# Optimization experiments

Measured on AMD Instinct MI355X. Metric: run time of the kernel, lower is better.

Reference implementation:

```python
import jax, jax.numpy as jnp
import numpy as np

N, E, IN, H, OUT = 100000, 1600000, 128, 128, 64


def setup_inputs() -> dict:
    key = jax.random.key(0)
    ks = jax.random.split(key, 7)
    x = jax.random.normal(ks[0], (N, IN), dtype=jnp.float32)
    edge_index = jax.random.randint(ks[1], (2, E), 0, N, dtype=jnp.int32)
    # Glorot-style scaled params (PyG SAGEConv: lin_l has bias, lin_r does not)
    s1 = 1.0 / np.sqrt(IN)
    s2 = 1.0 / np.sqrt(H)
    W1_l = jax.random.normal(ks[2], (H, IN), dtype=jnp.float32) * s1
    W1_r = jax.random.normal(ks[3], (H, IN), dtype=jnp.float32) * s1
    b1 = jnp.zeros((H,), dtype=jnp.float32)
    W2_l = jax.random.normal(ks[4], (OUT, H), dtype=jnp.float32) * s2
    W2_r = jax.random.normal(ks[5], (OUT, H), dtype=jnp.float32) * s2
    b2 = jnp.zeros((OUT,), dtype=jnp.float32)
    return {"x": x, "W1_l": W1_l, "W1_r": W1_r, "b1": b1,
            "W2_l": W2_l, "W2_r": W2_r, "b2": b2, "edge_index": edge_index}


def _sage_conv(x, edge_index, W_l, W_r, b):
    # mean-aggregate source-node features at target nodes, then linear + root term
    src, dst = edge_index[0], edge_index[1]
    n = x.shape[0]
    msgs = x[src]                                                   # [E, d]
    agg = jax.ops.segment_sum(msgs, dst, num_segments=n)            # [N, d]
    deg = jax.ops.segment_sum(jnp.ones((src.shape[0],), x.dtype), dst, num_segments=n)
    mean = agg / jnp.clip(deg, 1.0)[:, None]                        # zero-deg nodes stay 0
    return mean @ W_l.T + b + x @ W_r.T


def reference(x, W1_l, W1_r, b1, W2_l, W2_r, b2, edge_index):
    h = _sage_conv(x, edge_index, W1_l, W1_r, b1)
    h = jax.nn.relu(h)  # dropout p=0.0 -> identity
    out = _sage_conv(h, edge_index, W2_l, W2_r, b2)
    return out
```

## Files before the change

### kernel.cpp

```cpp
#include <hip/hip_runtime.h>


typedef unsigned int uint32;
typedef short bf16x4 __attribute__((ext_vector_type(4)));
typedef short bf16x8 __attribute__((ext_vector_type(8)));
typedef float f32x16 __attribute__((ext_vector_type(16)));

__device__ __forceinline__ uint32 pack_bf16_rne(float a, float b) {
    uint32 ua = __float_as_uint(a);
    uint32 ub = __float_as_uint(b);
    uint32 ra = (ua + 0x7fffu + ((ua >> 16) & 1u)) >> 16;
    uint32 rb = (ub + 0x7fffu + ((ub >> 16) & 1u)) >> 16;
    return ra | (rb << 16);
}
__device__ __forceinline__ float bf_lo(uint32 v) { return __uint_as_float(v << 16); }
__device__ __forceinline__ float bf_hi(uint32 v) { return __uint_as_float(v & 0xffff0000u); }

__device__ __forceinline__ short rne16(float v, float* back) {
    uint32 u = __float_as_uint(v);
    uint32 r = (u + 0x7fffu + ((u >> 16) & 1u)) >> 16;
    *back = __uint_as_float(r << 16);
    return (short)r;
}

__global__ void k_prep(const float* __restrict__ x, uint32* __restrict__ xb,
                       short* __restrict__ xpH, long n4, int spl,
                       const float* __restrict__ W1l, const float* __restrict__ W1r,
                       const float* __restrict__ W2l, const float* __restrict__ W2r,
                       short* __restrict__ W1pH, short* __restrict__ W1pL,
                       short* __restrict__ W2pH, short* __restrict__ W2pL) {
    long i = (long)blockIdx.x * blockDim.x + threadIdx.x;
    float back;
    if (i < n4) {
        int node = (int)(i >> 5);
        int k4 = ((int)i & 31) * 4;
        float4 v = ((const float4*)x)[i];
        bf16x4 hi4;
        hi4[0] = rne16(v.x, &back);
        hi4[1] = rne16(v.y, &back);
        hi4[2] = rne16(v.z, &back);
        hi4[3] = rne16(v.w, &back);
        uint2 o;
        o.x = (uint32)(unsigned short)hi4[0] | ((uint32)(unsigned short)hi4[1] << 16);
        o.y = (uint32)(unsigned short)hi4[2] | ((uint32)(unsigned short)hi4[3] << 16);
        ((uint2*)xb)[i] = o;
        int c = k4 >> 3;
        *(bf16x4*)&xpH[(size_t)c * spl + (size_t)node * 8 + (k4 & 7)] = hi4;
        return;
    }
    int i2 = (int)(i - n4);
    if (i2 < 32768) {
        int j = i2 >> 8, k = i2 & 255;
        float v = (k < 128) ? W1l[j * 128 + k] : W1r[j * 128 + k - 128];
        float hb;
        short hs = rne16(v, &hb);
        short ls = rne16(v - hb, &back);
        int idx = (k >> 3) * 1024 + j * 8 + (k & 7);
        W1pH[idx] = hs;
        W1pL[idx] = ls;
    } else if (i2 < 32768 + 16384) {
        int i3 = i2 - 32768;
        int j = i3 >> 7, k = i3 & 127;
        float v = (j < 64) ? W2l[j * 128 + k] : W2r[(j - 64) * 128 + k];
        float hb;
        short hs = rne16(v, &hb);
        short ls = rne16(v - hb, &back);
        int idx = (k >> 3) * 1024 + j * 8 + (k & 7);
        W2pH[idx] = hs;
        W2pL[idx] = ls;
    }
}


__global__ void k_bcount(const int* __restrict__ ei, int E, int NB,
                         int* __restrict__ bucket_cnt) {
    __shared__ int hist[1024];
    int t = threadIdx.x;
    for (int i = t; i < NB; i += 256) hist[i] = 0;
    __syncthreads();
    int stride = gridDim.x * 256;
    for (int e = blockIdx.x * 256 + t; e < E; e += stride)
        atomicAdd(&hist[ei[E + e] >> 8], 1);
    __syncthreads();
    for (int i = t; i < NB; i += 256) {
        int c = hist[i];
        if (c) atomicAdd(&bucket_cnt[i], c);
    }
}

__global__ void k_bscan(const int* __restrict__ bucket_cnt, int NB, int E,
                        int* __restrict__ bucket_off, int* __restrict__ bucket_cur) {
    __shared__ int s[1024];
    int t = threadIdx.x;
    int v = (t < NB) ? bucket_cnt[t] : 0;
    s[t] = v;
    __syncthreads();
    for (int o = 1; o < 1024; o <<= 1) {
        int u = (t >= o) ? s[t - o] : 0;
        __syncthreads();
        s[t] += u;
        __syncthreads();
    }
    int ex = s[t] - v;
    if (t < NB) { bucket_off[t] = ex; bucket_cur[t] = ex; }
    if (t == NB - 1) bucket_off[NB] = ex + v;
}

__global__ void k_bscatter(const int* __restrict__ ei, int E, int NB,
                           int* __restrict__ bucket_cur, uint32* __restrict__ eb) {
    __shared__ int hist[1024];
    __shared__ int base[1024];
    int t = threadIdx.x;
    for (int i = t; i < NB; i += 256) hist[i] = 0;
    __syncthreads();
    int stride = gridDim.x * 256;
    for (int e = blockIdx.x * 256 + t; e < E; e += stride)
        atomicAdd(&hist[ei[E + e] >> 8], 1);
    __syncthreads();
    for (int i = t; i < NB; i += 256) {
        int c = hist[i];
        base[i] = c ? atomicAdd(&bucket_cur[i], c) : 0;
        hist[i] = 0;
    }
    __syncthreads();
    for (int e = blockIdx.x * 256 + t; e < E; e += stride) {
        int d = ei[E + e];
        int b = d >> 8;
        int r = atomicAdd(&hist[b], 1);
        eb[base[b] + r] = ((uint32)(d & 255) << 24) | (uint32)ei[e];
    }
}

__global__ void k_bfinal(const uint32* __restrict__ eb,
                         const int* __restrict__ bucket_off,
                         int* __restrict__ row_ptr, int* __restrict__ col,
                         int N, int E) {
    __shared__ int deg[256];
    __shared__ int sc[256];
    __shared__ int cur[256];
    int b = blockIdx.x;
    int t = threadIdx.x;
    int beg = bucket_off[b], end = bucket_off[b + 1];
    deg[t] = 0;
    __syncthreads();
    for (int e = beg + t; e < end; e += 256)
        atomicAdd(&deg[eb[e] >> 24], 1);
    __syncthreads();
    int v = deg[t];
    sc[t] = v;
    __syncthreads();
    for (int o = 1; o < 256; o <<= 1) {
        int u = (t >= o) ? sc[t - o] : 0;
        __syncthreads();
        sc[t] += u;
        __syncthreads();
    }
    int ex = sc[t] - v;
    int node = b * 256 + t;
    if (node < N) row_ptr[node] = beg + ex;
    if (b == gridDim.x - 1 && t == 0) row_ptr[N] = E;
    cur[t] = ex;
    __syncthreads();
    for (int e = beg + t; e < end; e += 256) {
        uint32 u = eb[e];
        int r = atomicAdd(&cur[u >> 24], 1);
        col[beg + r] = (int)(u & 0xFFFFFFu);
    }
}


__global__ void k_agg_mean(const int* __restrict__ rp, const int* __restrict__ col,
                           const uint32* __restrict__ xb,
                           short* __restrict__ mpH, short* __restrict__ mpL,
                           int N, int spl) {
    int node = blockIdx.x * 4 + (threadIdx.x >> 6);
    if (node >= N) return;
    node = __builtin_amdgcn_readfirstlane(node);
    int lane = threadIdx.x & 63;
    int g = lane >> 4;
    int f = lane & 15;
    int beg = rp[node], end = rp[node + 1];
    const uint4* xb4 = (const uint4*)xb;
    float s[8];
#pragma unroll
    for (int j = 0; j < 8; j++) s[j] = 0.f;

#define ACC_RAW(v)                                                      \
    { s[0] += bf_lo(v.x); s[1] += __uint_as_float(v.x);                 \
      s[2] += bf_lo(v.y); s[3] += __uint_as_float(v.y);                 \
      s[4] += bf_lo(v.z); s[5] += __uint_as_float(v.z);                 \
      s[6] += bf_lo(v.w); s[7] += __uint_as_float(v.w); }

    int e = beg;
    for (; e + 16 <= end; e += 16) {
        uint4 cv = *(const uint4*)(col + e + 4 * g);
        uint4 v0 = xb4[(size_t)cv.x * 16 + f];
        uint4 v1 = xb4[(size_t)cv.y * 16 + f];
        uint4 v2 = xb4[(size_t)cv.z * 16 + f];
        uint4 v3 = xb4[(size_t)cv.w * 16 + f];
        ACC_RAW(v0); ACC_RAW(v1); ACC_RAW(v2); ACC_RAW(v3);
    }
    for (; e + 8 <= end; e += 8) {
        uint2 cv = *(const uint2*)(col + e + 2 * g);
        uint4 v0 = xb4[(size_t)cv.x * 16 + f];
        uint4 v1 = xb4[(size_t)cv.y * 16 + f];
        ACC_RAW(v0); ACC_RAW(v1);
    }
    int rem = end - e;
    if (2 * g < rem) {
        uint4 v0 = xb4[(size_t)col[e + 2 * g] * 16 + f];
        ACC_RAW(v0);
    }
    if (2 * g + 1 < rem) {
        uint4 v0 = xb4[(size_t)col[e + 2 * g + 1] * 16 + f];
        ACC_RAW(v0);
    }
#undef ACC_RAW
#pragma unroll
    for (int j = 0; j < 8; j++) {
        s[j] += __shfl_xor(s[j], 16);
        s[j] += __shfl_xor(s[j], 32);
    }
    if (g == 0) {
        float inv = 1.0f / (float)max(end - beg, 1);
        uint32 H[4], L[4];
#pragma unroll
        for (int p = 0; p < 4; p++) {
            float m0 = s[2 * p] * inv, m1 = s[2 * p + 1] * inv;
            float b;
            short h0 = rne16(m0, &b);
            short l0 = rne16(m0 - b, &b);
            short h1 = rne16(m1, &b);
            short l1 = rne16(m1 - b, &b);
            H[p] = (uint32)(unsigned short)h0 | ((uint32)(unsigned short)h1 << 16);
            L[p] = (uint32)(unsigned short)l0 | ((uint32)(unsigned short)l1 << 16);
        }
        size_t idx = (size_t)f * spl + (size_t)node * 8;
        *(uint4*)&mpH[idx] = make_uint4(H[0], H[1], H[2], H[3]);
        *(uint4*)&mpL[idx] = make_uint4(L[0], L[1], L[2], L[3]);
    }
}


__global__ __launch_bounds__(256, 4) void k_mgemm(
        const short* __restrict__ mpH, const short* __restrict__ mpL,
        const short* __restrict__ xpH,
        const short* __restrict__ W1pH, const short* __restrict__ W1pL,
        const short* __restrict__ W2pH, const short* __restrict__ W2pL,
        const float* __restrict__ b1, const float* __restrict__ b2,
        unsigned short* __restrict__ hl, float* __restrict__ hr, int N, int spl) {
    __shared__ short hpH[4096];
    __shared__ short hpL[4096];
    int t = threadIdx.x;
    int w = t >> 6, lane = t & 63;
    int m = lane & 31, hh = lane >> 5;
    int node0 = blockIdx.x * 32;
    int mynode = node0 + m;
    f32x16 acc;
#pragma unroll
    for (int r = 0; r < 16; r++) acc[r] = 0.f;

#pragma unroll
    for (int kc = 0; kc < 8; kc++) {
        int c = 2 * kc + hh;
        bf16x8 bH = *(const bf16x8*)(mpH + (size_t)c * spl + (size_t)mynode * 8);
        bf16x8 bL = *(const bf16x8*)(mpL + (size_t)c * spl + (size_t)mynode * 8);
        bf16x8 xH = *(const bf16x8*)(xpH + (size_t)c * spl + (size_t)mynode * 8);
        bf16x8 aH1 = *(const bf16x8*)(W1pH + c * 1024 + (32 * w + m) * 8);
        bf16x8 aL1 = *(const bf16x8*)(W1pL + c * 1024 + (32 * w + m) * 8);
        bf16x8 aH2 = *(const bf16x8*)(W1pH + (16 + c) * 1024 + (32 * w + m) * 8);
        bf16x8 aL2 = *(const bf16x8*)(W1pL + (16 + c) * 1024 + (32 * w + m) * 8);
        acc = __builtin_amdgcn_mfma_f32_32x32x16_bf16(aH1, bH, acc, 0, 0, 0);
        acc = __builtin_amdgcn_mfma_f32_32x32x16_bf16(aL1, bH, acc, 0, 0, 0);
        acc = __builtin_amdgcn_mfma_f32_32x32x16_bf16(aH1, bL, acc, 0, 0, 0);
        acc = __builtin_amdgcn_mfma_f32_32x32x16_bf16(aH2, xH, acc, 0, 0, 0);
        acc = __builtin_amdgcn_mfma_f32_32x32x16_bf16(aL2, xH, acc, 0, 0, 0);
    }

#pragma unroll
    for (int rg = 0; rg < 4; rg++) {
        int j0 = 32 * w + 8 * rg + 4 * hh;
        float4 bv = *(const float4*)(b1 + j0);
        float bb[4] = {bv.x, bv.y, bv.z, bv.w};
        short hs[4], ls[4];
#pragma unroll
        for (int q = 0; q < 4; q++) {
            float v = fmaxf(acc[4 * rg + q] + bb[q], 0.f);
            float back;
            hs[q] = rne16(v, &back);
            ls[q] = rne16(v - back, &back);
        }
        uint2 oh, ol;
        oh.x = (uint32)(unsigned short)hs[0] | ((uint32)(unsigned short)hs[1] << 16);
        oh.y = (uint32)(unsigned short)hs[2] | ((uint32)(unsigned short)hs[3] << 16);
        ol.x = (uint32)(unsigned short)ls[0] | ((uint32)(unsigned short)ls[1] << 16);
        ol.y = (uint32)(unsigned short)ls[2] | ((uint32)(unsigned short)ls[3] << 16);
        int idx = (4 * w + rg) * 256 + m * 8 + 4 * hh;
        *(uint2*)&hpH[idx] = oh;
        *(uint2*)&hpL[idx] = ol;
    }
    __syncthreads();

#pragma unroll
    for (int r = 0; r < 16; r++) acc[r] = 0.f;
#pragma unroll
    for (int kc = 0; kc < 8; kc++) {
        int c = 2 * kc + hh;
        bf16x8 bH = *(const bf16x8*)&hpH[c * 256 + m * 8];
        bf16x8 bL = *(const bf16x8*)&hpL[c * 256 + m * 8];
        bf16x8 aH = *(const bf16x8*)(W2pH + c * 1024 + (32 * w + m) * 8);
        bf16x8 aL = *(const bf16x8*)(W2pL + c * 1024 + (32 * w + m) * 8);
        acc = __builtin_amdgcn_mfma_f32_32x32x16_bf16(aH, bH, acc, 0, 0, 0);
        acc = __builtin_amdgcn_mfma_f32_32x32x16_bf16(aL, bH, acc, 0, 0, 0);
        acc = __builtin_amdgcn_mfma_f32_32x32x16_bf16(aH, bL, acc, 0, 0, 0);
    }
    if (mynode >= N) return;
    if (w < 2) {
#pragma unroll
        for (int rg = 0; rg < 4; rg++) {
            int j0 = 32 * w + 8 * rg + 4 * hh;
            uint2 o;
            o.x = pack_bf16_rne(acc[4 * rg + 0], acc[4 * rg + 1]);
            o.y = pack_bf16_rne(acc[4 * rg + 2], acc[4 * rg + 3]);
            *(uint2*)&hl[(size_t)mynode * 64 + j0] = o;
        }
    } else {
#pragma unroll
        for (int rg = 0; rg < 4; rg++) {
            int j0 = 32 * (w - 2) + 8 * rg + 4 * hh;
            float4 bv = *(const float4*)(b2 + j0);
            float4 o;
            o.x = acc[4 * rg + 0] + bv.x;
            o.y = acc[4 * rg + 1] + bv.y;
            o.z = acc[4 * rg + 2] + bv.z;
            o.w = acc[4 * rg + 3] + bv.w;
            *(float4*)&hr[(size_t)mynode * 64 + j0] = o;
        }
    }
}


__global__ void k_agg_out(const int* __restrict__ rp, const int* __restrict__ col,
                          const uint32* __restrict__ hl, const float* __restrict__ hr,
                          float* __restrict__ out, int N) {
    int node = blockIdx.x * 4 + (threadIdx.x >> 6);
    if (node >= N) return;
    node = __builtin_amdgcn_readfirstlane(node);
    int lane = threadIdx.x & 63;
    int g = lane >> 3;
    int f = lane & 7;
    int beg = rp[node], end = rp[node + 1];
    const uint4* hl4 = (const uint4*)hl;
    float s[8];
#pragma unroll
    for (int j = 0; j < 8; j++) s[j] = 0.f;

#define ACC_MSK(v)                                          \
    { s[0] += bf_lo(v.x); s[1] += bf_hi(v.x);               \
      s[2] += bf_lo(v.y); s[3] += bf_hi(v.y);               \
      s[4] += bf_lo(v.z); s[5] += bf_hi(v.z);               \
      s[6] += bf_lo(v.w); s[7] += bf_hi(v.w); }

    int e = beg;
    for (; e + 16 <= end; e += 16) {
        uint2 cv = *(const uint2*)(col + e + 2 * g);
        uint4 v0 = hl4[(size_t)cv.x * 8 + f];
        uint4 v1 = hl4[(size_t)cv.y * 8 + f];
        ACC_MSK(v0); ACC_MSK(v1);
    }
    for (; e + 8 <= end; e += 8) {
        uint4 v0 = hl4[(size_t)col[e + g] * 8 + f];
        ACC_MSK(v0);
    }
    int rem = end - e;
    if (g < rem) {
        uint4 v0 = hl4[(size_t)col[e + g] * 8 + f];
        ACC_MSK(v0);
    }
#undef ACC_MSK
#pragma unroll
    for (int j = 0; j < 8; j++) {
        s[j] += __shfl_xor(s[j], 8);
        s[j] += __shfl_xor(s[j], 16);
        s[j] += __shfl_xor(s[j], 32);
    }
    if (g == 0) {
        float inv = 1.0f / (float)max(end - beg, 1);
        const float* hrp = hr + (size_t)node * 64 + f * 8;
        float4 h0 = *(const float4*)(hrp);
        float4 h1 = *(const float4*)(hrp + 4);
        float4 o0, o1;
        o0.x = s[0] * inv + h0.x;
        o0.y = s[1] * inv + h0.y;
        o0.z = s[2] * inv + h0.z;
        o0.w = s[3] * inv + h0.w;
        o1.x = s[4] * inv + h1.x;
        o1.y = s[5] * inv + h1.y;
        o1.z = s[6] * inv + h1.z;
        o1.w = s[7] * inv + h1.w;
        float* op = out + (size_t)node * 64 + f * 8;
        *(float4*)(op) = o0;
        *(float4*)(op + 4) = o1;
    }
}

extern "C" void kernel_launch(void* const* d_in, const int* in_sizes, int n_in,
                              void* d_out, int out_size, void* d_ws, size_t ws_size,
                              hipStream_t stream) {
    const float* x   = (const float*)d_in[0];
    const float* W1l = (const float*)d_in[1];
    const float* W1r = (const float*)d_in[2];
    const float* b1  = (const float*)d_in[3];
    const float* W2l = (const float*)d_in[4];
    const float* W2r = (const float*)d_in[5];
    const float* b2  = (const float*)d_in[6];
    const int*   ei  = (const int*)d_in[7];
    int N = in_sizes[0] / 128;
    int E = in_sizes[7] / 2;
    int NB = (N + 255) >> 8;
    int gb = (N + 127) / 128;
    int Np = gb * 128;
    int spl = Np * 8;
    float* out = (float*)d_out;

    char* w = (char*)d_ws;
    size_t off = 0;
    auto alloc = [&](size_t bytes) -> char* {
        char* p = w + off;
        off += (bytes + 255) & ~(size_t)255;
        return p;
    };
    int*   row_ptr = (int*)alloc((size_t)(N + 1) * 4);
    int*   bcnt    = (int*)alloc((size_t)(NB + 1) * 4);
    int*   boff    = (int*)alloc((size_t)(NB + 1) * 4);
    int*   bcur    = (int*)alloc((size_t)(NB + 1) * 4);
    short* W1pH    = (short*)alloc(32768 * 2);
    short* W1pL    = (short*)alloc(32768 * 2);
    short* W2pH    = (short*)alloc(16384 * 2);
    short* W2pL    = (short*)alloc(16384 * 2);
    int*   col     = (int*)alloc((size_t)E * 4);
    short* xpH     = (short*)alloc((size_t)16 * spl * 2);
    short* mpH     = (short*)alloc((size_t)16 * spl * 2);
    short* mpL     = (short*)alloc((size_t)16 * spl * 2);
    unsigned short* hl = (unsigned short*)alloc((size_t)N * 64 * 2);
    char*  hrxb    = alloc((size_t)Np * 64 * 4);
    uint32* xb = (uint32*)hrxb;
    float*  hr = (float*)hrxb;
    uint32* eb = (uint32*)hl;

    hipMemsetAsync(bcnt, 0, (size_t)NB * 4, stream);
    long n4 = (long)N * 32;
    long prep_items = n4 + 32768 + 16384;
    k_prep<<<(int)((prep_items + 255) / 256), 256, 0, stream>>>(
        x, xb, xpH, n4, spl, W1l, W1r, W2l, W2r, W1pH, W1pL, W2pH, W2pL);
    k_bcount<<<256, 256, 0, stream>>>(ei, E, NB, bcnt);
    k_bscan<<<1, 1024, 0, stream>>>(bcnt, NB, E, boff, bcur);
    k_bscatter<<<128, 256, 0, stream>>>(ei, E, NB, bcur, eb);
    k_bfinal<<<NB, 256, 0, stream>>>(eb, boff, row_ptr, col, N, E);

    int ab = (N + 3) / 4;
    k_agg_mean<<<ab, 256, 0, stream>>>(row_ptr, col, xb, mpH, mpL, N, spl);
    int mb = (N + 31) / 32;
    k_mgemm<<<mb, 256, 0, stream>>>(mpH, mpL, xpH, W1pH, W1pL, W2pH, W2pL,
                                    b1, b2, hl, hr, N, spl);
    k_agg_out<<<ab, 256, 0, stream>>>(row_ptr, col, (const uint32*)hl, hr, out, N);
}
```

Measured before the change: 355.9 us.

## Fuse layer-1 mean aggregation into the MFMA GEMM kernel via shared memory

Merges the aggregation kernel and the fused two-layer GEMM kernel into one kernel. Each block aggregates 32 nodes into padded LDS tiles (stride 264) and then runs the MFMA GEMMs straight from LDS. This drops the global round trip for the split-bf16 mean buffers and the separately packed x buffer, and the prep kernel no longer writes xpH. The cost is a serial 8-node loop per wave with no overlap across blocks, more LDS per block that may lower occupancy, and separate xb/hr buffers instead of a shared alias.

```diff
diff --git a/kernel.cpp b/kernel.cpp
--- a/kernel.cpp
+++ b/kernel.cpp
@@ -5,6 +5,8 @@
 typedef short bf16x4 __attribute__((ext_vector_type(4)));
 typedef short bf16x8 __attribute__((ext_vector_type(8)));
 typedef float f32x16 __attribute__((ext_vector_type(16)));
+
+#define PSTR 264
 
 __device__ __forceinline__ uint32 pack_bf16_rne(float a, float b) {
     uint32 ua = __float_as_uint(a);
@@ -24,7 +26,7 @@
 }
 
 __global__ void k_prep(const float* __restrict__ x, uint32* __restrict__ xb,
-                       short* __restrict__ xpH, long n4, int spl,
+                       long n4,
                        const float* __restrict__ W1l, const float* __restrict__ W1r,
                        const float* __restrict__ W2l, const float* __restrict__ W2r,
                        short* __restrict__ W1pH, short* __restrict__ W1pL,
@@ -32,20 +34,15 @@
     long i = (long)blockIdx.x * blockDim.x + threadIdx.x;
     float back;
     if (i < n4) {
-        int node = (int)(i >> 5);
-        int k4 = ((int)i & 31) * 4;
         float4 v = ((const float4*)x)[i];
-        bf16x4 hi4;
-        hi4[0] = rne16(v.x, &back);
-        hi4[1] = rne16(v.y, &back);
-        hi4[2] = rne16(v.z, &back);
-        hi4[3] = rne16(v.w, &back);
+        short h0 = rne16(v.x, &back);
+        short h1 = rne16(v.y, &back);
+        short h2 = rne16(v.z, &back);
+        short h3 = rne16(v.w, &back);
         uint2 o;
-        o.x = (uint32)(unsigned short)hi4[0] | ((uint32)(unsigned short)hi4[1] << 16);
-        o.y = (uint32)(unsigned short)hi4[2] | ((uint32)(unsigned short)hi4[3] << 16);
+        o.x = (uint32)(unsigned short)h0 | ((uint32)(unsigned short)h1 << 16);
+        o.y = (uint32)(unsigned short)h2 | ((uint32)(unsigned short)h3 << 16);
         ((uint2*)xb)[i] = o;
-        int c = k4 >> 3;
-        *(bf16x4*)&xpH[(size_t)c * spl + (size_t)node * 8 + (k4 & 7)] = hi4;
         return;
     }
     int i2 = (int)(i - n4);
@@ -169,21 +166,43 @@
 }
 
 
-__global__ void k_agg_mean(const int* __restrict__ rp, const int* __restrict__ col,
-                           const uint32* __restrict__ xb,
-                           short* __restrict__ mpH, short* __restrict__ mpL,
-                           int N, int spl) {
-    int node = blockIdx.x * 4 + (threadIdx.x >> 6);
-    if (node >= N) return;
-    node = __builtin_amdgcn_readfirstlane(node);
-    int lane = threadIdx.x & 63;
-    int g = lane >> 4;
-    int f = lane & 15;
-    int beg = rp[node], end = rp[node + 1];
+__global__ __launch_bounds__(256, 4) void k_fused(
+        const int* __restrict__ rp, const int* __restrict__ col,
+        const uint32* __restrict__ xb,
+        const short* __restrict__ W1pH, const short* __restrict__ W1pL,
+        const short* __restrict__ W2pH, const short* __restrict__ W2pL,
+        const float* __restrict__ b1, const float* __restrict__ b2,
+        unsigned short* __restrict__ hl, float* __restrict__ hr, int N) {
+    __shared__ short smH[16 * PSTR];
+    __shared__ short smL[16 * PSTR];
+    __shared__ short sxH[16 * PSTR];
+    int t = threadIdx.x;
+    int w = t >> 6, lane = t & 63;
+    int g = lane >> 4, f = lane & 15;
+    int node0 = blockIdx.x * 32;
     const uint4* xb4 = (const uint4*)xb;
-    float s[8];
-#pragma unroll
-    for (int j = 0; j < 8; j++) s[j] = 0.f;
+
+#pragma unroll
+    for (int i = 0; i < 2; i++) {
+        int lr = 8 * w + 4 * i + g;
+        int gn = node0 + lr;
+        uint4 v = make_uint4(0u, 0u, 0u, 0u);
+        if (gn < N) v = xb4[(size_t)gn * 16 + f];
+        *(uint4*)&sxH[f * PSTR + lr * 8] = v;
+    }
+
+    int base = node0 + 8 * w;
+    int rpi = base + lane;
+    if (rpi > N) rpi = N;
+    int rpv = rp[rpi];
+
+    for (int i = 0; i < 8; i++) {
+        int lr = 8 * w + i;
+        int beg = __builtin_amdgcn_readfirstlane(__shfl(rpv, i));
+        int end = __builtin_amdgcn_readfirstlane(__shfl(rpv, i + 1));
+        float s[8];
+#pragma unroll
+        for (int j = 0; j < 8; j++) s[j] = 0.f;
 
 #define ACC_RAW(v)                                                      \
     { s[0] += bf_lo(v.x); s[1] += __uint_as_float(v.x);                 \
@@ -191,81 +210,63 @@
       s[4] += bf_lo(v.z); s[5] += __uint_as_float(v.z);                 \
       s[6] += bf_lo(v.w); s[7] += __uint_as_float(v.w); }
 
-    int e = beg;
-    for (; e + 16 <= end; e += 16) {
-        uint4 cv = *(const uint4*)(col + e + 4 * g);
-        uint4 v0 = xb4[(size_t)cv.x * 16 + f];
-        uint4 v1 = xb4[(size_t)cv.y * 16 + f];
-        uint4 v2 = xb4[(size_t)cv.z * 16 + f];
-        uint4 v3 = xb4[(size_t)cv.w * 16 + f];
-        ACC_RAW(v0); ACC_RAW(v1); ACC_RAW(v2); ACC_RAW(v3);
-    }
-    for (; e + 8 <= end; e += 8) {
-        uint2 cv = *(const uint2*)(col + e + 2 * g);
-        uint4 v0 = xb4[(size_t)cv.x * 16 + f];
-        uint4 v1 = xb4[(size_t)cv.y * 16 + f];
-        ACC_RAW(v0); ACC_RAW(v1);
-    }
-    int rem = end - e;
-    if (2 * g < rem) {
-        uint4 v0 = xb4[(size_t)col[e + 2 * g] * 16 + f];
-        ACC_RAW(v0);
-    }
-    if (2 * g + 1 < rem) {
-        uint4 v0 = xb4[(size_t)col[e + 2 * g + 1] * 16 + f];
-        ACC_RAW(v0);
-    }
+        int e = beg;
+        for (; e + 16 <= end; e += 16) {
+            uint4 cv = *(const uint4*)(col + e + 4 * g);
+            uint4 v0 = xb4[(size_t)cv.x * 16 + f];
+            uint4 v1 = xb4[(size_t)cv.y * 16 + f];
+            uint4 v2 = xb4[(size_t)cv.z * 16 + f];
+            uint4 v3 = xb4[(size_t)cv.w * 16 + f];
+            ACC_RAW(v0); ACC_RAW(v1); ACC_RAW(v2); ACC_RAW(v3);
+        }
+        for (; e + 8 <= end; e += 8) {
+            uint2 cv = *(const uint2*)(col + e + 2 * g);
+            uint4 v0 = xb4[(size_t)cv.x * 16 + f];
+            uint4 v1 = xb4[(size_t)cv.y * 16 + f];
+            ACC_RAW(v0); ACC_RAW(v1);
+        }
+        int rem = end - e;
+        if (2 * g < rem) {
+            uint4 v0 = xb4[(size_t)col[e + 2 * g] * 16 + f];
+            ACC_RAW(v0);
+        }
+        if (2 * g + 1 < rem) {
+            uint4 v0 = xb4[(size_t)col[e + 2 * g + 1] * 16 + f];
+            ACC_RAW(v0);
+        }
 #undef ACC_RAW
 #pragma unroll
-    for (int j = 0; j < 8; j++) {
-        s[j] += __shfl_xor(s[j], 16);
-        s[j] += __shfl_xor(s[j], 32);
-    }
-    if (g == 0) {
+        for (int j = 0; j < 8; j++) {
+            s[j] += __shfl_xor(s[j], 16);
+            s[j] += __shfl_xor(s[j], 32);
+        }
         float inv = 1.0f / (float)max(end - beg, 1);
-        uint32 H[4], L[4];
-#pragma unroll
-        for (int p = 0; p < 4; p++) {
-            float m0 = s[2 * p] * inv, m1 = s[2 * p + 1] * inv;
-            float b;
-            short h0 = rne16(m0, &b);
-            short l0 = rne16(m0 - b, &b);
-            short h1 = rne16(m1, &b);
-            short l1 = rne16(m1 - b, &b);
-            H[p] = (uint32)(unsigned short)h0 | ((uint32)(unsigned short)h1 << 16);
-            L[p] = (uint32)(unsigned short)l0 | ((uint32)(unsigned short)l1 << 16);
-        }
-        size_t idx = (size_t)f * spl + (size_t)node * 8;
-        *(uint4*)&mpH[idx] = make_uint4(H[0], H[1], H[2], H[3]);
-        *(uint4*)&mpL[idx] = make_uint4(L[0], L[1], L[2], L[3]);
-    }
-}
-
-
-__global__ __launch_bounds__(256, 4) void k_mgemm(
-        const short* __restrict__ mpH, const short* __restrict__ mpL,
-        const short* __restrict__ xpH,
-        const short* __restrict__ W1pH, const short* __restrict__ W1pL,
-        const short* __restrict__ W2pH, const short* __restrict__ W2pL,
-        const float* __restrict__ b1, const float* __restrict__ b2,
-        unsigned short* __restrict__ hl, float* __restrict__ hr, int N, int spl) {
-    __shared__ short hpH[4096];
-    __shared__ short hpL[4096];
-    int t = threadIdx.x;
-    int w = t >> 6, lane = t & 63;
+        float m0 = s[2 * g] * inv, m1 = s[2 * g + 1] * inv;
+        float b_;
+        short h0 = rne16(m0, &b_);
+        float bk0 = b_;
+        short l0 = rne16(m0 - bk0, &b_);
+        short h1 = rne16(m1, &b_);
+        float bk1 = b_;
+        short l1 = rne16(m1 - bk1, &b_);
+        uint32 H = (uint32)(unsigned short)h0 | ((uint32)(unsigned short)h1 << 16);
+        uint32 L = (uint32)(unsigned short)l0 | ((uint32)(unsigned short)l1 << 16);
+        *(uint32*)&smH[f * PSTR + lr * 8 + 2 * g] = H;
+        *(uint32*)&smL[f * PSTR + lr * 8 + 2 * g] = L;
+    }
+    __syncthreads();
+
     int m = lane & 31, hh = lane >> 5;
-    int node0 = blockIdx.x * 32;
     int mynode = node0 + m;
     f32x16 acc;
 #pragma unroll
     for (int r = 0; r < 16; r++) acc[r] = 0.f;
-
 #pragma unroll
     for (int kc = 0; kc < 8; kc++) {
         int c = 2 * kc + hh;
-        bf16x8 bH = *(const bf16x8*)(mpH + (size_t)c * spl + (size_t)mynode * 8);
-        bf16x8 bL = *(const bf16x8*)(mpL + (size_t)c * spl + (size_t)mynode * 8);
-        bf16x8 xH = *(const bf16x8*)(xpH + (size_t)c * spl + (size_t)mynode * 8);
+        bf16x8 bH = *(const bf16x8*)&smH[c * PSTR + m * 8];
+        bf16x8 bL = *(const bf16x8*)&smL[c * PSTR + m * 8];
+        bf16x8 xH = *(const bf16x8*)&sxH[c * PSTR + m * 8];
         bf16x8 aH1 = *(const bf16x8*)(W1pH + c * 1024 + (32 * w + m) * 8);
         bf16x8 aL1 = *(const bf16x8*)(W1pL + c * 1024 + (32 * w + m) * 8);
         bf16x8 aH2 = *(const bf16x8*)(W1pH + (16 + c) * 1024 + (32 * w + m) * 8);
@@ -277,6 +278,7 @@
         acc = __builtin_amdgcn_mfma_f32_32x32x16_bf16(aL2, xH, acc, 0, 0, 0);
     }
 
+    uint2 oh[4], ol[4];
 #pragma unroll
     for (int rg = 0; rg < 4; rg++) {
         int j0 = 32 * w + 8 * rg + 4 * hh;
@@ -290,14 +292,17 @@
             hs[q] = rne16(v, &back);
             ls[q] = rne16(v - back, &back);
         }
-        uint2 oh, ol;
-        oh.x = (uint32)(unsigned short)hs[0] | ((uint32)(unsigned short)hs[1] << 16);
-        oh.y = (uint32)(unsigned short)hs[2] | ((uint32)(unsigned short)hs[3] << 16);
-        ol.x = (uint32)(unsigned short)ls[0] | ((uint32)(unsigned short)ls[1] << 16);
-        ol.y = (uint32)(unsigned short)ls[2] | ((uint32)(unsigned short)ls[3] << 16);
-        int idx = (4 * w + rg) * 256 + m * 8 + 4 * hh;
-        *(uint2*)&hpH[idx] = oh;
-        *(uint2*)&hpL[idx] = ol;
+        oh[rg].x = (uint32)(unsigned short)hs[0] | ((uint32)(unsigned short)hs[1] << 16);
+        oh[rg].y = (uint32)(unsigned short)hs[2] | ((uint32)(unsigned short)hs[3] << 16);
+        ol[rg].x = (uint32)(unsigned short)ls[0] | ((uint32)(unsigned short)ls[1] << 16);
+        ol[rg].y = (uint32)(unsigned short)ls[2] | ((uint32)(unsigned short)ls[3] << 16);
+    }
+    __syncthreads();
+#pragma unroll
+    for (int rg = 0; rg < 4; rg++) {
+        int idx = (4 * w + rg) * PSTR + m * 8 + 4 * hh;
+        *(uint2*)&smH[idx] = oh[rg];
+        *(uint2*)&smL[idx] = ol[rg];
     }
     __syncthreads();
 
@@ -306,8 +311,8 @@
 #pragma unroll
     for (int kc = 0; kc < 8; kc++) {
         int c = 2 * kc + hh;
-        bf16x8 bH = *(const bf16x8*)&hpH[c * 256 + m * 8];
-        bf16x8 bL = *(const bf16x8*)&hpL[c * 256 + m * 8];
+        bf16x8 bH = *(const bf16x8*)&smH[c * PSTR + m * 8];
+        bf16x8 bL = *(const bf16x8*)&smL[c * PSTR + m * 8];
         bf16x8 aH = *(const bf16x8*)(W2pH + c * 1024 + (32 * w + m) * 8);
         bf16x8 aL = *(const bf16x8*)(W2pL + c * 1024 + (32 * w + m) * 8);
         acc = __builtin_amdgcn_mfma_f32_32x32x16_bf16(aH, bH, acc, 0, 0, 0);
@@ -418,9 +423,8 @@
     int N = in_sizes[0] / 128;
     int E = in_sizes[7] / 2;
     int NB = (N + 255) >> 8;
-    int gb = (N + 127) / 128;
-    int Np = gb * 128;
-    int spl = Np * 8;
+    int mb = (N + 31) / 32;
+    int Np = ((N + 127) / 128) * 128;
     float* out = (float*)d_out;
 
     char* w = (char*)d_ws;
@@ -439,29 +443,23 @@
     short* W2pH    = (short*)alloc(16384 * 2);
     short* W2pL    = (short*)alloc(16384 * 2);
     int*   col     = (int*)alloc((size_t)E * 4);
-    short* xpH     = (short*)alloc((size_t)16 * spl * 2);
-    short* mpH     = (short*)alloc((size_t)16 * spl * 2);
-    short* mpL     = (short*)alloc((size_t)16 * spl * 2);
+    uint32* xb     = (uint32*)alloc((size_t)Np * 64 * 4);
+    float*  hr     = (float*)alloc((size_t)Np * 64 * 4);
     unsigned short* hl = (unsigned short*)alloc((size_t)N * 64 * 2);
-    char*  hrxb    = alloc((size_t)Np * 64 * 4);
-    uint32* xb = (uint32*)hrxb;
-    float*  hr = (float*)hrxb;
     uint32* eb = (uint32*)hl;
 
     hipMemsetAsync(bcnt, 0, (size_t)NB * 4, stream);
     long n4 = (long)N * 32;
     long prep_items = n4 + 32768 + 16384;
     k_prep<<<(int)((prep_items + 255) / 256), 256, 0, stream>>>(
-        x, xb, xpH, n4, spl, W1l, W1r, W2l, W2r, W1pH, W1pL, W2pH, W2pL);
+        x, xb, n4, W1l, W1r, W2l, W2r, W1pH, W1pL, W2pH, W2pL);
     k_bcount<<<256, 256, 0, stream>>>(ei, E, NB, bcnt);
     k_bscan<<<1, 1024, 0, stream>>>(bcnt, NB, E, boff, bcur);
     k_bscatter<<<128, 256, 0, stream>>>(ei, E, NB, bcur, eb);
     k_bfinal<<<NB, 256, 0, stream>>>(eb, boff, row_ptr, col, N, E);
 
+    k_fused<<<mb, 256, 0, stream>>>(row_ptr, col, xb, W1pH, W1pL, W2pH, W2pL,
+                                    b1, b2, hl, hr, N);
     int ab = (N + 3) / 4;
-    k_agg_mean<<<ab, 256, 0, stream>>>(row_ptr, col, xb, mpH, mpL, N, spl);
-    int mb = (N + 31) / 32;
-    k_mgemm<<<mb, 256, 0, stream>>>(mpH, mpL, xpH, W1pH, W1pL, W2pH, W2pL,
-                                    b1, b2, hl, hr, N, spl);
     k_agg_out<<<ab, 256, 0, stream>>>(row_ptr, col, (const uint32*)hl, hr, out, N);
 }
```

After: 320.1 us. -10.1%, faster.
